# Performance work log

Measured on AMD Instinct MI355X. Metric: run time of the kernel, lower is better.

The kernel has to match this reference:

```python
import jax, jax.numpy as jnp
import numpy as np
from jax import lax

B, D, N, K, OUT = 32, 21, 1024, 32, 64
EPS_BN = 1e-5


def batchnorm(x, gamma, beta):
    # NCHW batchnorm, training-mode batch stats (biased variance), as torch does
    mean = jnp.mean(x, axis=(0, 2, 3), keepdims=True)
    var = jnp.mean((x - mean) ** 2, axis=(0, 2, 3), keepdims=True)
    xn = (x - mean) * lax.rsqrt(var + EPS_BN)
    return xn * gamma[None, :, None, None] + beta[None, :, None, None]


def setup_inputs() -> dict:
    key = jax.random.key(0)
    ks = jax.random.split(key, 4)
    x = jax.random.normal(ks[0], (B, D, N), dtype=jnp.float32)
    idx_base = jnp.arange(B, dtype=jnp.int64 if jax.config.jax_enable_x64 else jnp.int32).reshape(B, 1, 1)
    # kaiming-ish fan_in init for 1x1 convs (leaky relu a=0.2)
    gain = float(np.sqrt(2.0 / (1 + 0.2 ** 2)))
    w_dist = jax.random.normal(ks[1], (1, 1), dtype=jnp.float32) * gain  # Conv2d(1,1,1)
    w_gm = jax.random.normal(ks[2], (1, K), dtype=jnp.float32) * (gain / np.sqrt(K))  # Conv2d(k,1,1)
    w_up = jax.random.normal(ks[3], (OUT, D), dtype=jnp.float32) * (gain / np.sqrt(D))  # Conv2d(D,OUT,1)
    return {
        "x": x, "idx_base": idx_base,
        "w_dist": w_dist, "g1": jnp.ones((1,), jnp.float32), "b1": jnp.zeros((1,), jnp.float32),
        "w_gm": w_gm, "g2": jnp.ones((1,), jnp.float32), "b2": jnp.zeros((1,), jnp.float32),
        "w_up": w_up, "g3": jnp.ones((OUT,), jnp.float32), "b3": jnp.zeros((OUT,), jnp.float32),
    }


def reference(x, idx_base, w_dist, g1, b1, w_gm, g2, b2, w_up, g3, b3):
    Bs, Dd, Nn = x.shape
    Kk = w_gm.shape[1]
    xt = jnp.swapaxes(x, 1, 2)  # [B,N,D]
    xx = jnp.sum(x * x, axis=1)  # [B,N]
    inner = jnp.einsum('bnd,bmd->bnm', xt, xt)  # [B,N,N]
    # pairwise = -||xi-xj||^2
    pd = 2.0 * inner - xx[:, :, None] - xx[:, None, :]
    neg_dist, idx = lax.top_k(pd, Kk)  # [B,N,K]
    dist = -neg_dist  # positive squared distances
    # idx_base is arange(B).reshape(B,1,1); torch uses arange(B)*N offsets
    flat_idx = (idx + idx_base * Nn).reshape(-1)
    graph_feat = xt.reshape(Bs * Nn, Dd)[flat_idx].reshape(Bs, Nn, Kk, Dd)  # [B,N,K,D]
    gm = jnp.einsum('bnkd,bnjd->bnkj', graph_feat, graph_feat)  # [B,N,K,K]
    sub = gm[..., 0:1]  # [B,N,K,1] inner prods with self-neighbor
    sgm = sub * jnp.swapaxes(sub, -1, -2)  # [B,N,K,K]
    norm = jnp.sqrt(jnp.sum(sgm * sgm, axis=1, keepdims=True))  # F.normalize over dim=1
    sgm = sgm / jnp.maximum(norm, 1e-12)
    # NCHW layouts
    dist_n = dist[:, None, :, :]  # [B,1,N,K]
    gm2 = jnp.transpose(sgm, (0, 3, 1, 2))  # [B,K,N,K]
    feat_c = jnp.broadcast_to(xt[:, :, None, :], (Bs, Nn, Kk, Dd))
    feat_c = jnp.transpose(feat_c, (0, 3, 1, 2))  # [B,D,N,K]
    feat_n = jnp.transpose(graph_feat, (0, 3, 1, 2))  # [B,D,N,K]
    # dist_ff: 1x1 conv (scalar) + BN + sigmoid
    w1 = jax.nn.sigmoid(batchnorm(dist_n * w_dist[0, 0], g1, b1))  # [B,1,N,K]
    # gm2m_ff: 1x1 conv K->1 + BN + sigmoid
    gm_red = jnp.einsum('c,bchw->bhw', w_gm[0], gm2)[:, None]  # [B,1,N,K]
    w2 = jax.nn.sigmoid(batchnorm(gm_red, g2, b2))
    gate = w1 * w2
    feat = gate * feat_n + (1.0 - gate) * feat_c  # [B,D,N,K]
    up = jnp.einsum('oc,bchw->bohw', w_up, feat)  # [B,OUT,N,K]
    up = batchnorm(up, g3, b3)
    up = jnp.where(up >= 0, up, 0.02 * up)  # LeakyReLU(0.02)
    return jnp.mean(up, axis=-1)  # [B,OUT,N]
```

## Files before the change

kernel.cpp:

```cpp
#include <hip/hip_runtime.h>
#include <hip/hip_bf16.h>
#include <math.h>

#define BATCH 32
#define DFEAT 21
#define NPTS 1024
#define KSEL 32
#define NOUT 64

typedef unsigned long long u64;

__device__ __forceinline__ unsigned ord32(float f) {
    unsigned u = __float_as_uint(f);
    return ((int)u >= 0) ? (u | 0x80000000u) : ~u;
}
__device__ __forceinline__ float iord32(unsigned u) {
    unsigned s = (u & 0x80000000u) ? (u & 0x7FFFFFFFu) : ~u;
    return __uint_as_float(s);
}
__device__ __forceinline__ u64 mkkey(unsigned o, int m) {
    return ((u64)o << 32) | (unsigned)(~m);
}

template <int R>
__device__ __forceinline__ void sort2_desc(u64* A, u64* B, int lane) {
    const int NEL = R * 64;
    #pragma unroll
    for (int k = 2; k <= NEL; k <<= 1) {
        #pragma unroll
        for (int j = k >> 1; j >= 1; j >>= 1) {
            if (j >= 64) {
                const int rj = j >> 6;
                #pragma unroll
                for (int i = 0; i < R; ++i) {
                    if ((i & rj) == 0) {
                        const int e = lane + 64 * i;
                        const bool wm = ((e & k) == 0);
                        u64 x = A[i], y = A[i ^ rj];
                        u64 mx = x > y ? x : y, mn = x > y ? y : x;
                        A[i] = wm ? mx : mn; A[i ^ rj] = wm ? mn : mx;
                        x = B[i]; y = B[i ^ rj];
                        mx = x > y ? x : y; mn = x > y ? y : x;
                        B[i] = wm ? mx : mn; B[i ^ rj] = wm ? mn : mx;
                    }
                }
            } else {
                #pragma unroll
                for (int i = 0; i < R; ++i) {
                    const int e = lane + 64 * i;
                    const bool wm = ((e & j) == 0) == ((e & k) == 0);
                    const u64 oa = __shfl_xor(A[i], j);
                    const u64 ob = __shfl_xor(B[i], j);
                    const u64 mxa = A[i] > oa ? A[i] : oa;
                    const u64 mna = A[i] > oa ? oa : A[i];
                    A[i] = wm ? mxa : mna;
                    const u64 mxb = B[i] > ob ? B[i] : ob;
                    const u64 mnb = B[i] > ob ? ob : B[i];
                    B[i] = wm ? mxb : mnb;
                }
            }
        }
    }
}

__device__ __noinline__ u64 knn_fallback(const float* xs, const float* xxs,
                                         int n, int lane) {
    const float4* xs4  = (const float4*)xs;
    const float4* xxs4 = (const float4*)xxs;
    float4 acc[4];
    #pragma unroll
    for (int c = 0; c < 4; ++c) acc[c] = make_float4(0.f, 0.f, 0.f, 0.f);
    for (int d = 0; d < DFEAT; ++d) {
        const float xnd = xs[d * NPTS + n];
        #pragma unroll
        for (int c = 0; c < 4; ++c) {
            const float4 t = xs4[d * 256 + c * 64 + lane];
            acc[c].x = fmaf(t.x, xnd, acc[c].x);
            acc[c].y = fmaf(t.y, xnd, acc[c].y);
            acc[c].z = fmaf(t.z, xnd, acc[c].z);
            acc[c].w = fmaf(t.w, xnd, acc[c].w);
        }
    }
    const float xxn = xxs[n];
    unsigned ord[16];
    #pragma unroll
    for (int c = 0; c < 4; ++c) {
        const float4 xm = xxs4[c * 64 + lane];
        ord[c * 4 + 0] = ord32((2.f * acc[c].x - xxn) - xm.x);
        ord[c * 4 + 1] = ord32((2.f * acc[c].y - xxn) - xm.y);
        ord[c * 4 + 2] = ord32((2.f * acc[c].z - xxn) - xm.z);
        ord[c * 4 + 3] = ord32((2.f * acc[c].w - xxn) - xm.w);
    }
    u64 W = ~0ULL, win = 0ULL;
    for (int it = 0; it < 32; ++it) {
        u64 best = 0ULL;
        #pragma unroll
        for (int i = 0; i < 16; ++i) {
            const int m = (i >> 2) * 256 + lane * 4 + (i & 3);
            const u64 k = mkkey(ord[i], m);
            if (k < W && k > best) best = k;
        }
        #pragma unroll
        for (int off = 32; off >= 1; off >>= 1) {
            const u64 o = __shfl_xor(best, off);
            best = o > best ? o : best;
        }
        win = (lane == it) ? best : win;
        W = best;
    }
    return win;
}

__global__ __launch_bounds__(1024)
__attribute__((amdgpu_waves_per_eu(4, 4)))
void knn_kernel(
        const float* __restrict__ x,
        int* __restrict__ idx_ws, float* __restrict__ dist_ws,
        float* __restrict__ sub_ws) {
    extern __shared__ float smem[];
    float* xs  = smem;
    float* xxs = smem + DFEAT * NPTS;
    u64* cand  = (u64*)(smem + (DFEAT + 1) * NPTS);

    const int tid  = threadIdx.x;
    const int lane = tid & 63;
    const int w    = tid >> 6;
    const int b      = blockIdx.x >> 3;
    const int nchunk = blockIdx.x & 7;

    const float* xb = x + (size_t)b * DFEAT * NPTS;
    for (int i = tid; i < DFEAT * NPTS; i += 1024) xs[i] = xb[i];
    __syncthreads();
    {
        float s = 0.f;
        #pragma unroll
        for (int d = 0; d < DFEAT; ++d) { float v = xs[d * NPTS + tid]; s = fmaf(v, v, s); }
        xxs[tid] = s;
    }
    __syncthreads();

    u64* cwA = cand + (w * 2 + 0) * 128;
    u64* cwB = cand + (w * 2 + 1) * 128;
    const float4* xs4  = (const float4*)xs;
    const float4* xxs4 = (const float4*)xxs;

    const int nbase = nchunk * 128 + w * 8;

    for (int rp = 0; rp < 4; ++rp) {
        const int na = nbase + rp * 2;
        const int nb = na + 1;

        float4 accA[4], accB[4];
        #pragma unroll
        for (int c = 0; c < 4; ++c) {
            accA[c] = make_float4(0.f, 0.f, 0.f, 0.f);
            accB[c] = make_float4(0.f, 0.f, 0.f, 0.f);
        }
        for (int d = 0; d < DFEAT; ++d) {
            const float2 xn2 = *(const float2*)(xs + d * NPTS + na);
            const float xda = xn2.x;
            const float xdb = xn2.y;
            #pragma unroll
            for (int c = 0; c < 4; ++c) {
                const float4 t = xs4[d * 256 + c * 64 + lane];
                accA[c].x = fmaf(t.x, xda, accA[c].x);
                accA[c].y = fmaf(t.y, xda, accA[c].y);
                accA[c].z = fmaf(t.z, xda, accA[c].z);
                accA[c].w = fmaf(t.w, xda, accA[c].w);
                accB[c].x = fmaf(t.x, xdb, accB[c].x);
                accB[c].y = fmaf(t.y, xdb, accB[c].y);
                accB[c].z = fmaf(t.z, xdb, accB[c].z);
                accB[c].w = fmaf(t.w, xdb, accB[c].w);
            }
        }
        const float xxna = xxs[na], xxnb = xxs[nb];
        unsigned ordA[16], ordB[16];
        #pragma unroll
        for (int c = 0; c < 4; ++c) {
            const float4 xm = xxs4[c * 64 + lane];
            ordA[c * 4 + 0] = ord32((2.f * accA[c].x - xxna) - xm.x);
            ordA[c * 4 + 1] = ord32((2.f * accA[c].y - xxna) - xm.y);
            ordA[c * 4 + 2] = ord32((2.f * accA[c].z - xxna) - xm.z);
            ordA[c * 4 + 3] = ord32((2.f * accA[c].w - xxna) - xm.w);
            ordB[c * 4 + 0] = ord32((2.f * accB[c].x - xxnb) - xm.x);
            ordB[c * 4 + 1] = ord32((2.f * accB[c].y - xxnb) - xm.y);
            ordB[c * 4 + 2] = ord32((2.f * accB[c].z - xxnb) - xm.z);
            ordB[c * 4 + 3] = ord32((2.f * accB[c].w - xxnb) - xm.w);
        }

        unsigned va = ordA[0], vb = ordB[0];
        #pragma unroll
        for (int i = 1; i < 16; ++i) {
            va = ordA[i] > va ? ordA[i] : va;
            vb = ordB[i] > vb ? ordB[i] : vb;
        }

        #pragma unroll
        for (int kk = 2; kk <= 64; kk <<= 1) {
            #pragma unroll
            for (int j = kk >> 1; j >= 1; j >>= 1) {
                const unsigned oa = __shfl_xor(va, j);
                const unsigned ob = __shfl_xor(vb, j);
                const bool up      = ((lane & kk) == 0);
                const bool upper   = ((lane & j) != 0);
                const bool takeMax = (upper == up);
                va = (takeMax ? (oa > va) : (oa < va)) ? oa : va;
                vb = (takeMax ? (ob > vb) : (ob < vb)) ? ob : vb;
            }
        }
        const unsigned Ta = __shfl(va, 32);
        const unsigned Tb = __shfl(vb, 32);

        int ca = 0, cb = 0;
        #pragma unroll
        for (int i = 0; i < 16; ++i) {
            ca += (ordA[i] >= Ta) ? 1 : 0;
            cb += (ordB[i] >= Tb) ? 1 : 0;
        }
        int sa = ca, sb = cb;
        #pragma unroll
        for (int off = 1; off < 64; off <<= 1) {
            const int t2a = __shfl_up(sa, off);
            const int t2b = __shfl_up(sb, off);
            if (lane >= off) { sa += t2a; sb += t2b; }
        }
        const int baseA = sa - ca, baseB = sb - cb;
        const int CtA = __shfl(sa, 63), CtB = __shfl(sb, 63);

        {
            int p = baseA;
            #pragma unroll
            for (int i = 0; i < 16; ++i) {
                const int m = (i >> 2) * 256 + lane * 4 + (i & 3);
                if (ordA[i] >= Ta) { if (p < 128) cwA[p] = mkkey(ordA[i], m); ++p; }
            }
            p = baseB;
            #pragma unroll
            for (int i = 0; i < 16; ++i) {
                const int m = (i >> 2) * 256 + lane * 4 + (i & 3);
                if (ordB[i] >= Tb) { if (p < 128) cwB[p] = mkkey(ordB[i], m); ++p; }
            }
        }
        __asm__ volatile("s_waitcnt lgkmcnt(0)" ::: "memory");

        u64 keyA, keyB;
        if (CtA <= 128 && CtB <= 128) {
            if (CtA <= 64 && CtB <= 64) {
                u64 a0 = (lane < CtA) ? cwA[lane] : 0ULL;
                u64 b0 = (lane < CtB) ? cwB[lane] : 0ULL;
                sort2_desc<1>(&a0, &b0, lane);
                keyA = a0; keyB = b0;
            } else {
                u64 a[2], bb[2];
                #pragma unroll
                for (int i = 0; i < 2; ++i) {
                    const int ci = lane + 64 * i;
                    a[i]  = (ci < CtA) ? cwA[ci] : 0ULL;
                    bb[i] = (ci < CtB) ? cwB[ci] : 0ULL;
                }
                sort2_desc<2>(a, bb, lane);
                keyA = a[0]; keyB = bb[0];
            }
        } else {
            keyA = knn_fallback(xs, xxs, na, lane);
            keyB = knn_fallback(xs, xxs, nb, lane);
        }

        const int   mA = (int)(~(unsigned)keyA);
        const int   mB = (int)(~(unsigned)keyB);
        const float pdA = iord32((unsigned)(keyA >> 32));
        const float pdB = iord32((unsigned)(keyB >> 32));
        if (lane < KSEL) {
            const size_t oA = ((size_t)(b * NPTS + na)) * KSEL + lane;
            const size_t oB = ((size_t)(b * NPTS + nb)) * KSEL + lane;
            idx_ws[oA]  = mA;          idx_ws[oB]  = mB;
            dist_ws[oA] = -pdA;        dist_ws[oB] = -pdB;
            sub_ws[oA]  = 0.5f * ((pdA + xxs[mA]) + xxna);
            sub_ws[oB]  = 0.5f * ((pdB + xxs[mB]) + xxnb);
        }
    }
}

__global__ __launch_bounds__(256) void norm_part_kernel(
        const float* __restrict__ sub_ws, float* __restrict__ npart) {
    __shared__ float qS[128 * 33];
    const int tid = threadIdx.x;
    const int bc = blockIdx.x;
    const float* sb = sub_ws + (size_t)bc * 128 * KSEL;
    for (int i = tid; i < 128 * 32; i += 256) {
        const float v = sb[i];
        qS[(i >> 5) * 33 + (i & 31)] = v * v;
    }
    __syncthreads();
    const int k = tid >> 3, jg = tid & 7;
    float a0 = 0.f, a1 = 0.f, a2 = 0.f, a3 = 0.f;
    for (int n = 0; n < 128; ++n) {
        const float qk = qS[n * 33 + k];
        a0 = fmaf(qk, qS[n * 33 + jg], a0);
        a1 = fmaf(qk, qS[n * 33 + jg + 8], a1);
        a2 = fmaf(qk, qS[n * 33 + jg + 16], a2);
        a3 = fmaf(qk, qS[n * 33 + jg + 24], a3);
    }
    float* op = npart + (size_t)bc * 1024 + k * 32 + jg;
    op[0] = a0; op[8] = a1; op[16] = a2; op[24] = a3;
}

__global__ __launch_bounds__(1024) void norm_combine_kernel(
        const float* __restrict__ npart, float* __restrict__ recip_ws) {
    const int b = blockIdx.x, t = threadIdx.x;
    float s = 0.f;
    #pragma unroll
    for (int c = 0; c < 8; ++c)
        s += npart[((size_t)(b * 8 + c)) * 1024 + t];
    recip_ws[(size_t)b * NPTS + t] = 1.0f / fmaxf(sqrtf(s), 1e-12f);
}

__global__ __launch_bounds__(256) void gmred_kernel(
        const float* __restrict__ sub_ws, const float* __restrict__ dist_ws,
        const float* __restrict__ recip_ws, const float* __restrict__ w_gm,
        float* __restrict__ gmred_ws, double* __restrict__ part12) {
    __shared__ float subS[32 * 32];
    __shared__ float subWS[32 * 32];
    __shared__ double redS[4][4];

    const int tid = threadIdx.x;
    const int b   = blockIdx.x >> 5;
    const int n0  = (blockIdx.x & 31) * 32;

    {
        const float4 wv = ((const float4*)w_gm)[tid & 7];
        const float4 sv = ((const float4*)(sub_ws + ((size_t)(b * NPTS + n0)) * KSEL))[tid];
        ((float4*)subS)[tid] = sv;
        float4 t;
        t.x = sv.x * wv.x; t.y = sv.y * wv.y; t.z = sv.z * wv.z; t.w = sv.w * wv.w;
        ((float4*)subWS)[tid] = t;
    }
    const int k = tid & 31, rg = tid >> 5;
    float rk[32];
    {
        const float4* rp = (const float4*)(recip_ws + (size_t)b * NPTS + k * 32);
        #pragma unroll
        for (int c4 = 0; c4 < 8; ++c4) {
            const float4 v = rp[c4];
            rk[c4 * 4 + 0] = v.x; rk[c4 * 4 + 1] = v.y;
            rk[c4 * 4 + 2] = v.z; rk[c4 * 4 + 3] = v.w;
        }
    }
    __syncthreads();

    float sacc[4] = {0.f, 0.f, 0.f, 0.f};
    const float4* swp = (const float4*)subWS;
    #pragma unroll
    for (int c4 = 0; c4 < 8; ++c4) {
        #pragma unroll
        for (int i = 0; i < 4; ++i) {
            const float4 sw = swp[(rg * 4 + i) * 8 + c4];
            sacc[i] = fmaf(sw.x, rk[c4 * 4 + 0], sacc[i]);
            sacc[i] = fmaf(sw.y, rk[c4 * 4 + 1], sacc[i]);
            sacc[i] = fmaf(sw.z, rk[c4 * 4 + 2], sacc[i]);
            sacc[i] = fmaf(sw.w, rk[c4 * 4 + 3], sacc[i]);
        }
    }

    double s1 = 0, s2 = 0, s3 = 0, s4 = 0;
    #pragma unroll
    for (int i = 0; i < 4; ++i) {
        const int rl = rg * 4 + i;
        const float g = subS[rl * 32 + k] * sacc[i];
        const size_t row = (size_t)(b * NPTS + n0 + rl);
        gmred_ws[row * KSEL + k] = g;
        const float dv = dist_ws[row * KSEL + k];
        s1 += (double)dv; s2 = fma((double)dv, (double)dv, s2);
        s3 += (double)g;  s4 = fma((double)g, (double)g, s4);
    }
    #pragma unroll
    for (int off = 32; off >= 1; off >>= 1) {
        s1 += __shfl_xor(s1, off);
        s2 += __shfl_xor(s2, off);
        s3 += __shfl_xor(s3, off);
        s4 += __shfl_xor(s4, off);
    }
    if ((tid & 63) == 0) {
        const int wv = tid >> 6;
        redS[wv][0] = s1; redS[wv][1] = s2; redS[wv][2] = s3; redS[wv][3] = s4;
    }
    __syncthreads();
    if (tid == 0) {
        double a0 = 0, a1 = 0, a2 = 0, a3 = 0;
        #pragma unroll
        for (int wv = 0; wv < 4; ++wv) {
            a0 += redS[wv][0]; a1 += redS[wv][1]; a2 += redS[wv][2]; a3 += redS[wv][3];
        }
        part12[(size_t)blockIdx.x * 4 + 0] = a0;
        part12[(size_t)blockIdx.x * 4 + 1] = a1;
        part12[(size_t)blockIdx.x * 4 + 2] = a2;
        part12[(size_t)blockIdx.x * 4 + 3] = a3;
    }
}

__global__ __launch_bounds__(256) void uc_kernel(
        const float* __restrict__ x, const float* __restrict__ w_up,
        float* __restrict__ uc_ws) {
    __shared__ float wS[NOUT * DFEAT];
    const int tid = threadIdx.x, lane = tid & 63, w = tid >> 6;
    const int b  = blockIdx.x >> 4;
    const int n0 = (blockIdx.x & 15) * 64;
    for (int i = tid; i < NOUT * DFEAT; i += 256) wS[i] = w_up[i];
    __syncthreads();
    float wr[DFEAT];
    #pragma unroll
    for (int d = 0; d < DFEAT; ++d) wr[d] = wS[lane * DFEAT + d];
    const float* xb = x + (size_t)b * DFEAT * NPTS;
    for (int g = 0; g < 4; ++g) {
        const int nn = __builtin_amdgcn_readfirstlane(n0 + w * 16 + g * 4);
        float a0 = 0.f, a1 = 0.f, a2 = 0.f, a3 = 0.f;
        #pragma unroll
        for (int d = 0; d < DFEAT; ++d) {
            const float* xp = xb + d * NPTS + nn;
            const float wd = wr[d];
            a0 = fmaf(wd, xp[0], a0);
            a1 = fmaf(wd, xp[1], a1);
            a2 = fmaf(wd, xp[2], a2);
            a3 = fmaf(wd, xp[3], a3);
        }
        float* op = uc_ws + ((size_t)(b * NPTS) + nn) * NOUT + lane;
        op[0 * NOUT] = a0; op[1 * NOUT] = a1; op[2 * NOUT] = a2; op[3 * NOUT] = a3;
    }
}

__global__ __launch_bounds__(256) void reduce12_kernel(
        const double* __restrict__ part12, int nblocks,
        const float* __restrict__ w_dist,
        const float* __restrict__ g1, const float* __restrict__ b1,
        const float* __restrict__ g2, const float* __restrict__ b2,
        float* __restrict__ consts) {
    __shared__ double S[256][4];
    const int t = threadIdx.x;
    double a0 = 0, a1 = 0, a2 = 0, a3 = 0;
    for (int i = t; i < nblocks; i += 256) {
        a0 += part12[(size_t)i * 4 + 0];
        a1 += part12[(size_t)i * 4 + 1];
        a2 += part12[(size_t)i * 4 + 2];
        a3 += part12[(size_t)i * 4 + 3];
    }
    S[t][0] = a0; S[t][1] = a1; S[t][2] = a2; S[t][3] = a3;
    __syncthreads();
    for (int off = 128; off >= 1; off >>= 1) {
        if (t < off) {
            S[t][0] += S[t + off][0]; S[t][1] += S[t + off][1];
            S[t][2] += S[t + off][2]; S[t][3] += S[t + off][3];
        }
        __syncthreads();
    }
    if (t == 0) {
        const double M = (double)BATCH * NPTS * KSEL;
        const double E1 = S[0][0] / M, E2 = S[0][1] / M;
        const double wd = (double)w_dist[0];
        const double mean1 = wd * E1;
        const double var1  = wd * wd * (E2 - E1 * E1);
        const double istd1 = 1.0 / sqrt(var1 + 1e-5);
        consts[0] = (float)(wd * istd1 * (double)g1[0]);
        consts[1] = (float)((double)b1[0] - mean1 * istd1 * (double)g1[0]);
        const double F1 = S[0][2] / M, F2 = S[0][3] / M;
        const double var2  = F2 - F1 * F1;
        const double istd2 = 1.0 / sqrt(var2 + 1e-5);
        consts[2] = (float)(istd2 * (double)g2[0]);
        consts[3] = (float)((double)b2[0] - F1 * istd2 * (double)g2[0]);
    }
}

__global__ __launch_bounds__(256) void gate_kernel(
        const float* __restrict__ dist_ws, const float* __restrict__ gmred_ws,
        const float* __restrict__ consts, float* __restrict__ gate_ws) {
    const int i = blockIdx.x * 256 + threadIdx.x;
    const float A1 = consts[0], C1 = consts[1], A2 = consts[2], C2 = consts[3];
    const float4 dv = ((const float4*)dist_ws)[i];
    const float4 gv = ((const float4*)gmred_ws)[i];
    float4 r;
    r.x = (1.f / (1.f + __expf(-fmaf(dv.x, A1, C1)))) * (1.f / (1.f + __expf(-fmaf(gv.x, A2, C2))));
    r.y = (1.f / (1.f + __expf(-fmaf(dv.y, A1, C1)))) * (1.f / (1.f + __expf(-fmaf(gv.y, A2, C2))));
    r.z = (1.f / (1.f + __expf(-fmaf(dv.z, A1, C1)))) * (1.f / (1.f + __expf(-fmaf(gv.z, A2, C2))));
    r.w = (1.f / (1.f + __expf(-fmaf(dv.w, A1, C1)))) * (1.f / (1.f + __expf(-fmaf(gv.w, A2, C2))));
    ((float4*)gate_ws)[i] = r;
}

__global__ __launch_bounds__(256) void gate_stats_kernel(
        const float* __restrict__ gate_ws, const int* __restrict__ idx_ws,
        const float* __restrict__ uc_ws, double* __restrict__ part3) {
    const int tid = threadIdx.x, lane = tid & 63, w = tid >> 6;
    const int bid = blockIdx.x;
    const int lbid = (bid & 7) * 256 + (bid >> 3);
    const int b  = lbid >> 6;
    const int n0 = (lbid & 63) * 16;
    const float* ucb = uc_ws + (size_t)b * NPTS * NOUT;
    double sum = 0.0, ssq = 0.0;
    for (int rr = 0; rr < 4; ++rr) {
        const int n = __builtin_amdgcn_readfirstlane(n0 + w * 4 + rr);
        const int row = b * NPTS + n;
        const float* gp = gate_ws + (size_t)row * KSEL;
        const int*   ip = idx_ws  + (size_t)row * KSEL;
        const float ucr = ucb[(size_t)n * NOUT + lane];
        float fs = 0.f, fq = 0.f;
        #pragma unroll
        for (int k = 0; k < KSEL; ++k) {
            const float gk = gp[k];
            const int   jk = ip[k];
            const float ucn = ucb[(size_t)jk * NOUT + lane];
            const float up  = fmaf(gk, ucn - ucr, ucr);
            fs += up;
            fq = fmaf(up, up, fq);
        }
        sum += (double)fs; ssq += (double)fq;
    }
    __shared__ double p3[4][NOUT][2];
    p3[w][lane][0] = sum; p3[w][lane][1] = ssq;
    __syncthreads();
    if (w == 0) {
        const double s = p3[0][lane][0] + p3[1][lane][0] + p3[2][lane][0] + p3[3][lane][0];
        const double q = p3[0][lane][1] + p3[1][lane][1] + p3[2][lane][1] + p3[3][lane][1];
        part3[((size_t)bid * NOUT + lane) * 2 + 0] = s;
        part3[((size_t)bid * NOUT + lane) * 2 + 1] = q;
    }
}

__global__ __launch_bounds__(256) void reduce3_kernel(
        const double* __restrict__ part3,
        const float* __restrict__ g3, const float* __restrict__ b3,
        float* __restrict__ consts3) {
    const int o = blockIdx.x, t = threadIdx.x;
    double s = 0, q = 0;
    for (int i = t; i < 2048; i += 256) {
        s += part3[((size_t)i * NOUT + o) * 2 + 0];
        q += part3[((size_t)i * NOUT + o) * 2 + 1];
    }
    __shared__ double S[256][2];
    S[t][0] = s; S[t][1] = q;
    __syncthreads();
    for (int off = 128; off >= 1; off >>= 1) {
        if (t < off) { S[t][0] += S[t + off][0]; S[t][1] += S[t + off][1]; }
        __syncthreads();
    }
    if (t == 0) {
        const double M = (double)BATCH * NPTS * KSEL;
        const double mean = S[0][0] / M;
        const double var  = S[0][1] / M - mean * mean;
        const double istd = 1.0 / sqrt(var + 1e-5);
        consts3[o]        = (float)(istd * (double)g3[o]);
        consts3[64 + o]   = (float)((double)b3[o] - mean * istd * (double)g3[o]);
    }
}

__global__ __launch_bounds__(256) void final_kernel(
        const float* __restrict__ gate_ws, const int* __restrict__ idx_ws,
        const float* __restrict__ uc_ws, const float* __restrict__ consts3,
        float* __restrict__ out) {
    __shared__ float buf[16 * 65];
    const int tid = threadIdx.x, lane = tid & 63, w = tid >> 6;
    const int bid = blockIdx.x;
    const int lbid = (bid & 7) * 256 + (bid >> 3);
    const int b  = lbid >> 6;
    const int n0 = (lbid & 63) * 16;
    const float* ucb = uc_ws + (size_t)b * NPTS * NOUT;
    const float A = consts3[lane], C = consts3[64 + lane];
    for (int rr = 0; rr < 4; ++rr) {
        const int n = __builtin_amdgcn_readfirstlane(n0 + w * 4 + rr);
        const int row = b * NPTS + n;
        const float* gp = gate_ws + (size_t)row * KSEL;
        const int*   ip = idx_ws  + (size_t)row * KSEL;
        const float ucr = ucb[(size_t)n * NOUT + lane];
        float acc = 0.f;
        #pragma unroll
        for (int k = 0; k < KSEL; ++k) {
            const float gk = gp[k];
            const int   jk = ip[k];
            const float ucn = ucb[(size_t)jk * NOUT + lane];
            const float up  = fmaf(gk, ucn - ucr, ucr);
            float z = fmaf(up, A, C);
            z = (z >= 0.f) ? z : 0.02f * z;
            acc += z;
        }
        buf[(w * 4 + rr) * 65 + lane] = acc * (1.f / 32.f);
    }
    __syncthreads();
    const int o = tid >> 2, g = tid & 3;
    float4 v;
    v.x = buf[(g * 4 + 0) * 65 + o];
    v.y = buf[(g * 4 + 1) * 65 + o];
    v.z = buf[(g * 4 + 2) * 65 + o];
    v.w = buf[(g * 4 + 3) * 65 + o];
    float4* op = (float4*)(out + (size_t)b * NOUT * NPTS + (size_t)o * NPTS + n0);
    op[g] = v;
}

extern "C" void kernel_launch(void* const* d_in, const int* in_sizes, int n_in,
                              void* d_out, int out_size, void* d_ws, size_t ws_size,
                              hipStream_t stream) {
    const float* x      = (const float*)d_in[0];
    const float* w_dist = (const float*)d_in[2];
    const float* g1     = (const float*)d_in[3];
    const float* b1     = (const float*)d_in[4];
    const float* w_gm   = (const float*)d_in[5];
    const float* g2     = (const float*)d_in[6];
    const float* b2     = (const float*)d_in[7];
    const float* w_up   = (const float*)d_in[8];
    const float* g3     = (const float*)d_in[9];
    const float* b3     = (const float*)d_in[10];
    float* out = (float*)d_out;

    char* ws = (char*)d_ws;
    int*    idx_ws   = (int*)(ws + 0);
    float*  dist_ws  = (float*)(ws + ((size_t)4 << 20));
    float*  sub_ws   = (float*)(ws + ((size_t)8 << 20));
    float*  gmred_ws = (float*)(ws + ((size_t)12 << 20));
    float*  gate_ws  = (float*)(ws + ((size_t)16 << 20));
    float*  uc_ws    = (float*)(ws + ((size_t)20 << 20));
    float*  recip_ws = (float*)(ws + ((size_t)28 << 20));
    double* part12   = (double*)(ws + ((size_t)28 << 20) + 0x20000);
    float*  consts   = (float*)(ws + ((size_t)28 << 20) + 0x60000);
    float*  consts3  = consts + 8;
    float*  npart    = gate_ws;
    double* part3    = (double*)gmred_ws;

    const int knn_lds = (DFEAT + 1) * NPTS * 4 + 16 * 2 * 128 * 8;

    knn_kernel<<<dim3(256), dim3(1024), knn_lds, stream>>>(x, idx_ws, dist_ws, sub_ws);
    norm_part_kernel<<<dim3(256), dim3(256), 0, stream>>>(sub_ws, npart);
    norm_combine_kernel<<<dim3(32), dim3(1024), 0, stream>>>(npart, recip_ws);
    uc_kernel<<<dim3(512), dim3(256), 0, stream>>>(x, w_up, uc_ws);
    gmred_kernel<<<dim3(1024), dim3(256), 0, stream>>>(sub_ws, dist_ws, recip_ws, w_gm,
                                                       gmred_ws, part12);
    reduce12_kernel<<<dim3(1), dim3(256), 0, stream>>>(part12, 1024, w_dist, g1, b1, g2, b2,
                                                       consts);
    gate_kernel<<<dim3(1024), dim3(256), 0, stream>>>(dist_ws, gmred_ws, consts, gate_ws);
    gate_stats_kernel<<<dim3(2048), dim3(256), 0, stream>>>(gate_ws, idx_ws, uc_ws, part3);
    reduce3_kernel<<<dim3(64), dim3(256), 0, stream>>>(part3, g3, b3, consts3);
    final_kernel<<<dim3(2048), dim3(256), 0, stream>>>(gate_ws, idx_ws, uc_ws, consts3, out);
}
```

Baseline: 139.0 us.

## Register-tile KNN distances over 4 rows with LDS exchange; fuse gate into stats

The KNN kernel now lets each pair of waves compute a 4-query-row by half-column tile, so each loaded xs element feeds more FMAs. Partial ordered keys are swapped through a shared-memory buffer so each wave still holds full rows for top-k. The shared arrays become static, and x is loaded with float4. The gate computation moves into gate_stats_kernel, which removes one launch and a round trip through gate_ws, and part3 now aliases sub_ws. The cost is extra barriers and LDS exchange traffic per iteration, plus higher register pressure.

```diff
diff --git a/kernel.cpp b/kernel.cpp
--- a/kernel.cpp
+++ b/kernel.cpp
@@ -111,25 +111,42 @@
     return win;
 }
 
+#define ORD8(O, A0, A1, XXN) \
+    O[0] = ord32((2.f * A0.x - XXN) - xm0.x); \
+    O[1] = ord32((2.f * A0.y - XXN) - xm0.y); \
+    O[2] = ord32((2.f * A0.z - XXN) - xm0.z); \
+    O[3] = ord32((2.f * A0.w - XXN) - xm0.w); \
+    O[4] = ord32((2.f * A1.x - XXN) - xm1.x); \
+    O[5] = ord32((2.f * A1.y - XXN) - xm1.y); \
+    O[6] = ord32((2.f * A1.z - XXN) - xm1.z); \
+    O[7] = ord32((2.f * A1.w - XXN) - xm1.w);
+
 __global__ __launch_bounds__(1024)
 __attribute__((amdgpu_waves_per_eu(4, 4)))
 void knn_kernel(
         const float* __restrict__ x,
         int* __restrict__ idx_ws, float* __restrict__ dist_ws,
         float* __restrict__ sub_ws) {
-    extern __shared__ float smem[];
-    float* xs  = smem;
-    float* xxs = smem + DFEAT * NPTS;
-    u64* cand  = (u64*)(smem + (DFEAT + 1) * NPTS);
+    __shared__ __align__(16) float xs[DFEAT * NPTS];
+    __shared__ __align__(16) float xxs[NPTS];
+    __shared__ __align__(16) unsigned exbuf[8 * 4 * 512];
+
+    u64*   cand = (u64*)exbuf;
+    uint4* EX4  = (uint4*)exbuf;
 
     const int tid  = threadIdx.x;
     const int lane = tid & 63;
     const int w    = tid >> 6;
+    const int q    = w >> 1;
+    const int h    = w & 1;
     const int b      = blockIdx.x >> 3;
     const int nchunk = blockIdx.x & 7;
 
-    const float* xb = x + (size_t)b * DFEAT * NPTS;
-    for (int i = tid; i < DFEAT * NPTS; i += 1024) xs[i] = xb[i];
+    {
+        const float4* xb4 = (const float4*)(x + (size_t)b * DFEAT * NPTS);
+        float4* xsw = (float4*)xs;
+        for (int i = tid; i < DFEAT * 256; i += 1024) xsw[i] = xb4[i];
+    }
     __syncthreads();
     {
         float s = 0.f;
@@ -137,56 +154,91 @@
         for (int d = 0; d < DFEAT; ++d) { float v = xs[d * NPTS + tid]; s = fmaf(v, v, s); }
         xxs[tid] = s;
     }
-    __syncthreads();
 
     u64* cwA = cand + (w * 2 + 0) * 128;
     u64* cwB = cand + (w * 2 + 1) * 128;
     const float4* xs4  = (const float4*)xs;
     const float4* xxs4 = (const float4*)xxs;
-
-    const int nbase = nchunk * 128 + w * 8;
-
-    for (int rp = 0; rp < 4; ++rp) {
-        const int na = nbase + rp * 2;
+    const int nbase = nchunk * 128 + q * 16;
+    const int hoff  = h * 128;
+
+    for (int it = 0; it < 4; ++it) {
+        __syncthreads();
+        const int n0 = nbase + it * 4;
+
+        float4 a00 = make_float4(0.f,0.f,0.f,0.f), a01 = a00;
+        float4 a10 = a00, a11 = a00, a20 = a00, a21 = a00, a30 = a00, a31 = a00;
+        for (int d = 0; d < DFEAT; ++d) {
+            const float4 xn = *(const float4*)(xs + d * NPTS + n0);
+            const float4 t0 = xs4[d * 256 + hoff + lane];
+            const float4 t1 = xs4[d * 256 + hoff + 64 + lane];
+            a00.x = fmaf(t0.x, xn.x, a00.x); a00.y = fmaf(t0.y, xn.x, a00.y);
+            a00.z = fmaf(t0.z, xn.x, a00.z); a00.w = fmaf(t0.w, xn.x, a00.w);
+            a01.x = fmaf(t1.x, xn.x, a01.x); a01.y = fmaf(t1.y, xn.x, a01.y);
+            a01.z = fmaf(t1.z, xn.x, a01.z); a01.w = fmaf(t1.w, xn.x, a01.w);
+            a10.x = fmaf(t0.x, xn.y, a10.x); a10.y = fmaf(t0.y, xn.y, a10.y);
+            a10.z = fmaf(t0.z, xn.y, a10.z); a10.w = fmaf(t0.w, xn.y, a10.w);
+            a11.x = fmaf(t1.x, xn.y, a11.x); a11.y = fmaf(t1.y, xn.y, a11.y);
+            a11.z = fmaf(t1.z, xn.y, a11.z); a11.w = fmaf(t1.w, xn.y, a11.w);
+            a20.x = fmaf(t0.x, xn.z, a20.x); a20.y = fmaf(t0.y, xn.z, a20.y);
+            a20.z = fmaf(t0.z, xn.z, a20.z); a20.w = fmaf(t0.w, xn.z, a20.w);
+            a21.x = fmaf(t1.x, xn.z, a21.x); a21.y = fmaf(t1.y, xn.z, a21.y);
+            a21.z = fmaf(t1.z, xn.z, a21.z); a21.w = fmaf(t1.w, xn.z, a21.w);
+            a30.x = fmaf(t0.x, xn.w, a30.x); a30.y = fmaf(t0.y, xn.w, a30.y);
+            a30.z = fmaf(t0.z, xn.w, a30.z); a30.w = fmaf(t0.w, xn.w, a30.w);
+            a31.x = fmaf(t1.x, xn.w, a31.x); a31.y = fmaf(t1.y, xn.w, a31.y);
+            a31.z = fmaf(t1.z, xn.w, a31.z); a31.w = fmaf(t1.w, xn.w, a31.w);
+        }
+        const float4 xm0 = xxs4[hoff + lane];
+        const float4 xm1 = xxs4[hoff + 64 + lane];
+        const float4 xxn = *(const float4*)(xxs + n0);
+        unsigned o0[8], o1[8], o2[8], o3[8];
+        ORD8(o0, a00, a01, xxn.x)
+        ORD8(o1, a10, a11, xxn.y)
+        ORD8(o2, a20, a21, xxn.z)
+        ORD8(o3, a30, a31, xxn.w)
+
+        {
+            const int sp = 2 - 2 * h;
+            const unsigned* pa = (h == 0) ? o2 : o0;
+            const unsigned* pb = (h == 0) ? o3 : o1;
+            uint4 v;
+            v.x = pa[0]; v.y = pa[1]; v.z = pa[2]; v.w = pa[3];
+            EX4[(q * 4 + sp) * 128 + lane] = v;
+            v.x = pa[4]; v.y = pa[5]; v.z = pa[6]; v.w = pa[7];
+            EX4[(q * 4 + sp) * 128 + 64 + lane] = v;
+            v.x = pb[0]; v.y = pb[1]; v.z = pb[2]; v.w = pb[3];
+            EX4[(q * 4 + sp + 1) * 128 + lane] = v;
+            v.x = pb[4]; v.y = pb[5]; v.z = pb[6]; v.w = pb[7];
+            EX4[(q * 4 + sp + 1) * 128 + 64 + lane] = v;
+        }
+        __syncthreads();
+
+        const int na = n0 + 2 * h;
         const int nb = na + 1;
-
-        float4 accA[4], accB[4];
-        #pragma unroll
-        for (int c = 0; c < 4; ++c) {
-            accA[c] = make_float4(0.f, 0.f, 0.f, 0.f);
-            accB[c] = make_float4(0.f, 0.f, 0.f, 0.f);
-        }
-        for (int d = 0; d < DFEAT; ++d) {
-            const float2 xn2 = *(const float2*)(xs + d * NPTS + na);
-            const float xda = xn2.x;
-            const float xdb = xn2.y;
+        unsigned ordA[16], ordB[16];
+        {
+            const unsigned* oa = (h == 0) ? o0 : o2;
+            const unsigned* ob = (h == 0) ? o1 : o3;
+            const int ownbase = h * 8;
+            const int pbase   = 8 - h * 8;
             #pragma unroll
-            for (int c = 0; c < 4; ++c) {
-                const float4 t = xs4[d * 256 + c * 64 + lane];
-                accA[c].x = fmaf(t.x, xda, accA[c].x);
-                accA[c].y = fmaf(t.y, xda, accA[c].y);
-                accA[c].z = fmaf(t.z, xda, accA[c].z);
-                accA[c].w = fmaf(t.w, xda, accA[c].w);
-                accB[c].x = fmaf(t.x, xdb, accB[c].x);
-                accB[c].y = fmaf(t.y, xdb, accB[c].y);
-                accB[c].z = fmaf(t.z, xdb, accB[c].z);
-                accB[c].w = fmaf(t.w, xdb, accB[c].w);
-            }
-        }
-        const float xxna = xxs[na], xxnb = xxs[nb];
-        unsigned ordA[16], ordB[16];
-        #pragma unroll
-        for (int c = 0; c < 4; ++c) {
-            const float4 xm = xxs4[c * 64 + lane];
-            ordA[c * 4 + 0] = ord32((2.f * accA[c].x - xxna) - xm.x);
-            ordA[c * 4 + 1] = ord32((2.f * accA[c].y - xxna) - xm.y);
-            ordA[c * 4 + 2] = ord32((2.f * accA[c].z - xxna) - xm.z);
-            ordA[c * 4 + 3] = ord32((2.f * accA[c].w - xxna) - xm.w);
-            ordB[c * 4 + 0] = ord32((2.f * accB[c].x - xxnb) - xm.x);
-            ordB[c * 4 + 1] = ord32((2.f * accB[c].y - xxnb) - xm.y);
-            ordB[c * 4 + 2] = ord32((2.f * accB[c].z - xxnb) - xm.z);
-            ordB[c * 4 + 3] = ord32((2.f * accB[c].w - xxnb) - xm.w);
-        }
+            for (int i = 0; i < 8; ++i) { ordA[ownbase + i] = oa[i]; ordB[ownbase + i] = ob[i]; }
+            uint4 p;
+            p = EX4[(q * 4 + 2 * h) * 128 + lane];
+            ordA[pbase + 0] = p.x; ordA[pbase + 1] = p.y;
+            ordA[pbase + 2] = p.z; ordA[pbase + 3] = p.w;
+            p = EX4[(q * 4 + 2 * h) * 128 + 64 + lane];
+            ordA[pbase + 4] = p.x; ordA[pbase + 5] = p.y;
+            ordA[pbase + 6] = p.z; ordA[pbase + 7] = p.w;
+            p = EX4[(q * 4 + 2 * h + 1) * 128 + lane];
+            ordB[pbase + 0] = p.x; ordB[pbase + 1] = p.y;
+            ordB[pbase + 2] = p.z; ordB[pbase + 3] = p.w;
+            p = EX4[(q * 4 + 2 * h + 1) * 128 + 64 + lane];
+            ordB[pbase + 4] = p.x; ordB[pbase + 5] = p.y;
+            ordB[pbase + 6] = p.z; ordB[pbase + 7] = p.w;
+        }
+        __syncthreads();
 
         unsigned va = ordA[0], vb = ordB[0];
         #pragma unroll
@@ -194,7 +246,6 @@
             va = ordA[i] > va ? ordA[i] : va;
             vb = ordB[i] > vb ? ordB[i] : vb;
         }
-
         #pragma unroll
         for (int kk = 2; kk <= 64; kk <<= 1) {
             #pragma unroll
@@ -270,6 +321,8 @@
         const int   mB = (int)(~(unsigned)keyB);
         const float pdA = iord32((unsigned)(keyA >> 32));
         const float pdB = iord32((unsigned)(keyB >> 32));
+        const float xxna = (h == 0) ? xxn.x : xxn.z;
+        const float xxnb = (h == 0) ? xxn.y : xxn.w;
         if (lane < KSEL) {
             const size_t oA = ((size_t)(b * NPTS + na)) * KSEL + lane;
             const size_t oB = ((size_t)(b * NPTS + nb)) * KSEL + lane;
@@ -469,41 +522,40 @@
     }
 }
 
-__global__ __launch_bounds__(256) void gate_kernel(
+__global__ __launch_bounds__(256) void gate_stats_kernel(
         const float* __restrict__ dist_ws, const float* __restrict__ gmred_ws,
-        const float* __restrict__ consts, float* __restrict__ gate_ws) {
-    const int i = blockIdx.x * 256 + threadIdx.x;
-    const float A1 = consts[0], C1 = consts[1], A2 = consts[2], C2 = consts[3];
-    const float4 dv = ((const float4*)dist_ws)[i];
-    const float4 gv = ((const float4*)gmred_ws)[i];
-    float4 r;
-    r.x = (1.f / (1.f + __expf(-fmaf(dv.x, A1, C1)))) * (1.f / (1.f + __expf(-fmaf(gv.x, A2, C2))));
-    r.y = (1.f / (1.f + __expf(-fmaf(dv.y, A1, C1)))) * (1.f / (1.f + __expf(-fmaf(gv.y, A2, C2))));
-    r.z = (1.f / (1.f + __expf(-fmaf(dv.z, A1, C1)))) * (1.f / (1.f + __expf(-fmaf(gv.z, A2, C2))));
-    r.w = (1.f / (1.f + __expf(-fmaf(dv.w, A1, C1)))) * (1.f / (1.f + __expf(-fmaf(gv.w, A2, C2))));
-    ((float4*)gate_ws)[i] = r;
-}
-
-__global__ __launch_bounds__(256) void gate_stats_kernel(
-        const float* __restrict__ gate_ws, const int* __restrict__ idx_ws,
-        const float* __restrict__ uc_ws, double* __restrict__ part3) {
+        const int* __restrict__ idx_ws, const float* __restrict__ uc_ws,
+        const float* __restrict__ consts,
+        float* __restrict__ gate_ws, double* __restrict__ part3) {
+    __shared__ float gS[4][32];
     const int tid = threadIdx.x, lane = tid & 63, w = tid >> 6;
     const int bid = blockIdx.x;
     const int lbid = (bid & 7) * 256 + (bid >> 3);
     const int b  = lbid >> 6;
     const int n0 = (lbid & 63) * 16;
+    const float A1 = consts[0], C1 = consts[1], A2 = consts[2], C2 = consts[3];
     const float* ucb = uc_ws + (size_t)b * NPTS * NOUT;
     double sum = 0.0, ssq = 0.0;
     for (int rr = 0; rr < 4; ++rr) {
         const int n = __builtin_amdgcn_readfirstlane(n0 + w * 4 + rr);
         const int row = b * NPTS + n;
-        const float* gp = gate_ws + (size_t)row * KSEL;
-        const int*   ip = idx_ws  + (size_t)row * KSEL;
+        if (lane < KSEL) {
+            const size_t rbase = (size_t)row * KSEL + lane;
+            const float dv = dist_ws[rbase];
+            const float gv = gmred_ws[rbase];
+            const float w1 = 1.f / (1.f + __expf(-fmaf(dv, A1, C1)));
+            const float w2 = 1.f / (1.f + __expf(-fmaf(gv, A2, C2)));
+            const float gate = w1 * w2;
+            gate_ws[rbase] = gate;
+            gS[w][lane] = gate;
+        }
+        __asm__ volatile("s_waitcnt lgkmcnt(0)" ::: "memory");
+        const int* ip = idx_ws + (size_t)row * KSEL;
         const float ucr = ucb[(size_t)n * NOUT + lane];
         float fs = 0.f, fq = 0.f;
         #pragma unroll
         for (int k = 0; k < KSEL; ++k) {
-            const float gk = gp[k];
+            const float gk = gS[w][k];
             const int   jk = ip[k];
             const float ucn = ucb[(size_t)jk * NOUT + lane];
             const float up  = fmaf(gk, ucn - ucr, ucr);
@@ -619,11 +671,9 @@
     float*  consts   = (float*)(ws + ((size_t)28 << 20) + 0x60000);
     float*  consts3  = consts + 8;
     float*  npart    = gate_ws;
-    double* part3    = (double*)gmred_ws;
-
-    const int knn_lds = (DFEAT + 1) * NPTS * 4 + 16 * 2 * 128 * 8;
-
-    knn_kernel<<<dim3(256), dim3(1024), knn_lds, stream>>>(x, idx_ws, dist_ws, sub_ws);
+    double* part3    = (double*)sub_ws;
+
+    knn_kernel<<<dim3(256), dim3(1024), 0, stream>>>(x, idx_ws, dist_ws, sub_ws);
     norm_part_kernel<<<dim3(256), dim3(256), 0, stream>>>(sub_ws, npart);
     norm_combine_kernel<<<dim3(32), dim3(1024), 0, stream>>>(npart, recip_ws);
     uc_kernel<<<dim3(512), dim3(256), 0, stream>>>(x, w_up, uc_ws);
@@ -631,8 +681,8 @@
                                                        gmred_ws, part12);
     reduce12_kernel<<<dim3(1), dim3(256), 0, stream>>>(part12, 1024, w_dist, g1, b1, g2, b2,
                                                        consts);
-    gate_kernel<<<dim3(1024), dim3(256), 0, stream>>>(dist_ws, gmred_ws, consts, gate_ws);
-    gate_stats_kernel<<<dim3(2048), dim3(256), 0, stream>>>(gate_ws, idx_ws, uc_ws, part3);
+    gate_stats_kernel<<<dim3(2048), dim3(256), 0, stream>>>(dist_ws, gmred_ws, idx_ws, uc_ws,
+                                                            consts, gate_ws, part3);
     reduce3_kernel<<<dim3(64), dim3(256), 0, stream>>>(part3, g3, b3, consts3);
     final_kernel<<<dim3(2048), dim3(256), 0, stream>>>(gate_ws, idx_ws, uc_ws, consts3, out);
 }
```

Result: slower. 339.4 us (+144.2%).
